# Optimization experiments

Hardware: AMD Instinct MI355X
Metric: run time of the kernel (lower is better)

The kernel has to match this reference:

```python
import jax, jax.numpy as jnp
import numpy as np

N = 131072   # utterances
D = 256      # embedding dim
C = 1024     # speakers (unique labels)


def setup_inputs() -> dict:
    key = jax.random.key(0)
    k1, k2 = jax.random.split(key)
    embeddings = jax.random.normal(k1, (N, D), dtype=jnp.float32)
    labels = jax.random.randint(k2, (N,), 0, C, dtype=jnp.int32)
    w = jnp.asarray(10.0, dtype=jnp.float32)
    b = jnp.asarray(-5.0, dtype=jnp.float32)
    return {"embeddings": embeddings, "labels": labels, "w": w, "b": b}


def reference(embeddings, labels, w, b):
    # Segment mean -> centroids [C, D]. With N >> C all labels occur, so
    # torch.unique(labels) == arange(C) and target == labels.
    sums = jax.ops.segment_sum(embeddings, labels, num_segments=C)
    counts = jax.ops.segment_sum(jnp.ones((embeddings.shape[0],), embeddings.dtype),
                                 labels, num_segments=C)
    centroids = sums / counts[:, None]
    # logits [N, C]
    logits = w * jnp.einsum('nd,cd->nc', embeddings, centroids) + b
    logp = jax.nn.log_softmax(logits, axis=-1)
    nll = -jnp.take_along_axis(logp, labels[:, None].astype(jnp.int32), axis=1)[:, 0]
    return jnp.mean(nll)
```

## Files before the change

### kernel.cpp

```cpp
#include <hip/hip_runtime.h>
#include <hip/hip_bf16.h>

#define NROWS 131072
#define DDIM  256
#define CDIM  1024

#define L2E 1.4426950408889634f
#define LN2 0.6931471805599453f

typedef short bf16x8 __attribute__((ext_vector_type(8)));
typedef float f32x4 __attribute__((ext_vector_type(4)));

__device__ __forceinline__ unsigned short f2b(float x) {
    unsigned int u = __builtin_bit_cast(unsigned int, x);
    u = (u + 0x7FFFu + ((u >> 16) & 1u)) >> 16;
    return (unsigned short)u;
}

__global__ void k_hist(const int* __restrict__ labels, int* __restrict__ hist) {
    const int i = blockIdx.x * 256 + threadIdx.x;
    atomicAdd(&hist[labels[i]], 1);
}

__global__ void k_scan(const int* __restrict__ hist, int* __restrict__ offsets) {
    __shared__ int tmp[CDIM];
    const int t = threadIdx.x;
    const int v = hist[t];
    tmp[t] = v;
    __syncthreads();
    for (int d = 1; d < CDIM; d <<= 1) {
        const int add = (t >= d) ? tmp[t - d] : 0;
        __syncthreads();
        tmp[t] += add;
        __syncthreads();
    }
    offsets[t] = tmp[t] - v;
    if (t == CDIM - 1) offsets[CDIM] = tmp[t];
}

__global__ void k_scatter(const int* __restrict__ labels, const int* __restrict__ offsets,
                          int* __restrict__ cursor, int* __restrict__ rowidx) {
    const int i = blockIdx.x * 256 + threadIdx.x;
    const int lab = labels[i];
    const int pos = atomicAdd(&cursor[lab], 1);
    rowidx[offsets[lab] + pos] = i;
}

__global__ void k_centroid(const float* __restrict__ emb, const int* __restrict__ rowidx,
                           const int* __restrict__ offsets, unsigned short* __restrict__ cent) {
    __shared__ f32x4 red[4][64];
    const int c = blockIdx.x;
    const int t = threadIdx.x;
    const int w = t >> 6;
    const int lane = t & 63;
    const int beg = offsets[c], end = offsets[c + 1];

    f32x4 acc = {0.0f, 0.0f, 0.0f, 0.0f};
    for (int i = beg + w * 2; i < end; i += 8) {
        const int row0 = rowidx[i];
        const int row1 = (i + 1 < end) ? rowidx[i + 1] : -1;
        const float4 v0 = *reinterpret_cast<const float4*>(emb + (size_t)row0 * DDIM + lane * 4);
        if (row1 >= 0) {
            const float4 v1 = *reinterpret_cast<const float4*>(emb + (size_t)row1 * DDIM + lane * 4);
            acc[0] += v1.x; acc[1] += v1.y; acc[2] += v1.z; acc[3] += v1.w;
        }
        acc[0] += v0.x; acc[1] += v0.y; acc[2] += v0.z; acc[3] += v0.w;
    }
    red[w][lane] = acc;
    __syncthreads();
    if (t < 64) {
        const f32x4 a0 = red[0][t], a1 = red[1][t], a2 = red[2][t], a3 = red[3][t];
        const float inv = 1.0f / (float)(end - beg);
        ushort4 h;
        h.x = f2b((a0[0] + a1[0] + a2[0] + a3[0]) * inv);
        h.y = f2b((a0[1] + a1[1] + a2[1] + a3[1]) * inv);
        h.z = f2b((a0[2] + a1[2] + a2[2] + a3[2]) * inv);
        h.w = f2b((a0[3] + a1[3] + a2[3] + a3[3]) * inv);
        *reinterpret_cast<ushort4*>(cent + c * DDIM + t * 4) = h;
    }
}

__launch_bounds__(256, 2)
__global__ void k_logits(const float* __restrict__ emb, const int* __restrict__ labels,
                         const unsigned short* __restrict__ cent, const float* __restrict__ wp,
                         float* __restrict__ nll_accum) {
    __shared__ unsigned short A_lds[64 * 256];
    __shared__ unsigned short B_lds[64 * 256];
    char* const Ab = reinterpret_cast<char*>(A_lds);
    char* const Bb = reinterpret_cast<char*>(B_lds);

    const float wscale = wp[0];
    const int t = threadIdx.x;
    const int wave = t >> 6;
    const int lane = t & 63;
    const int lg = lane >> 4;
    const int lr = lane & 15;
    const int rowbase = blockIdx.x * 64;

    for (int i = 0; i < 16; ++i) {
        const int flat = i * 1024 + t * 4;
        const int row = flat >> 8;
        const int k = flat & 255;
        const float4 v = *reinterpret_cast<const float4*>(emb + (size_t)(rowbase + row) * DDIM + k);
        ushort4 h;
        h.x = f2b(v.x); h.y = f2b(v.y); h.z = f2b(v.z); h.w = f2b(v.w);
        const int byte = ((row << 9) + (k << 1)) ^ ((row & 7) << 4);
        *reinterpret_cast<ushort4*>(Ab + byte) = h;
    }
    __syncthreads();

    bf16x8 af[8];
    {
        const int row = wave * 16 + lr;
#pragma unroll
        for (int kk = 0; kk < 8; ++kk) {
            const int byte = ((row << 9) + kk * 64 + lg * 16) ^ ((row & 7) << 4);
            af[kk] = *reinterpret_cast<const bf16x8*>(Ab + byte);
        }
    }

    float m[4], s[4], lv[4];
    int labs[4];
#pragma unroll
    for (int r = 0; r < 4; ++r) {
        m[r] = -1e30f; s[r] = 0.0f; lv[r] = 0.0f;
        labs[r] = labels[rowbase + wave * 16 + lg * 4 + r];
    }

    for (int cc = 0; cc < 16; ++cc) {
        __syncthreads();
        const unsigned short* src = cent + cc * (64 * 256);
        for (int i = 0; i < 8; ++i) {
            const int flat = i * 2048 + t * 8;
            const int col = flat >> 8;
            const int k = flat & 255;
            const uint4 v = *reinterpret_cast<const uint4*>(src + flat);
            const int byte = ((col << 9) + (k << 1)) ^ ((col & 7) << 4);
            *reinterpret_cast<uint4*>(Bb + byte) = v;
        }
        __syncthreads();

        float vals[4][4];
#pragma unroll
        for (int ct = 0; ct < 4; ++ct) {
            f32x4 acc = {0.0f, 0.0f, 0.0f, 0.0f};
            const int brow = ct * 16 + lr;
#pragma unroll
            for (int kk = 0; kk < 8; ++kk) {
                const int byte = ((brow << 9) + kk * 64 + lg * 16) ^ ((brow & 7) << 4);
                const bf16x8 bf = *reinterpret_cast<const bf16x8*>(Bb + byte);
                acc = __builtin_amdgcn_mfma_f32_16x16x32_bf16(af[kk], bf, acc, 0, 0, 0);
            }
            const int colg = cc * 64 + ct * 16 + lr;
#pragma unroll
            for (int r = 0; r < 4; ++r) {
                const float v = wscale * acc[r];
                vals[ct][r] = v;
                if (colg == labs[r]) lv[r] = v;
            }
        }
#pragma unroll
        for (int r = 0; r < 4; ++r) {
            const float cmax = fmaxf(fmaxf(vals[0][r], vals[1][r]),
                                     fmaxf(vals[2][r], vals[3][r]));
            const float mo = m[r];
            const float mn = fmaxf(mo, cmax);
            const float ssum = exp2f((vals[0][r] - mn) * L2E) + exp2f((vals[1][r] - mn) * L2E)
                             + exp2f((vals[2][r] - mn) * L2E) + exp2f((vals[3][r] - mn) * L2E);
            s[r] = s[r] * exp2f((mo - mn) * L2E) + ssum;
            m[r] = mn;
        }
    }

    float part = 0.0f;
#pragma unroll
    for (int r = 0; r < 4; ++r) {
        float mm = m[r], ss = s[r], ll = lv[r];
#pragma unroll
        for (int off = 1; off < 16; off <<= 1) {
            const float mo = __shfl_xor(mm, off, 64);
            const float so = __shfl_xor(ss, off, 64);
            const float lo = __shfl_xor(ll, off, 64);
            const float mn = fmaxf(mm, mo);
            ss = ss * exp2f((mm - mn) * L2E) + so * exp2f((mo - mn) * L2E);
            mm = mn;
            ll += lo;
        }
        if (lr == 0) {
            const float lse = mm + log2f(ss) * LN2;
            part += (lse - ll);
        }
    }
    if (lr == 0) atomicAdd(nll_accum, part * (1.0f / NROWS));
}

__global__ void k_final(const float* __restrict__ accum, float* __restrict__ out) {
    out[0] = accum[0];
}

extern "C" void kernel_launch(void* const* d_in, const int* in_sizes, int n_in,
                              void* d_out, int out_size, void* d_ws, size_t ws_size,
                              hipStream_t stream) {
    const float* emb = (const float*)d_in[0];
    const int* labels = (const int*)d_in[1];
    const float* wp = (const float*)d_in[2];
    float* out = (float*)d_out;

    int* hist = (int*)d_ws;
    int* cursor = (int*)((char*)d_ws + 4096);
    int* offsets = (int*)((char*)d_ws + 8192);
    float* accum = (float*)((char*)d_ws + 12544);
    int* rowidx = (int*)((char*)d_ws + 16384);
    unsigned short* cent = (unsigned short*)((char*)d_ws + 540672);

    hipMemsetAsync(d_ws, 0, 16384, stream);

    k_hist<<<NROWS / 256, 256, 0, stream>>>(labels, hist);
    k_scan<<<1, CDIM, 0, stream>>>(hist, offsets);
    k_scatter<<<NROWS / 256, 256, 0, stream>>>(labels, offsets, cursor, rowidx);
    k_centroid<<<CDIM, 256, 0, stream>>>(emb, rowidx, offsets, cent);
    k_logits<<<NROWS / 64, 256, 0, stream>>>(emb, labels, cent, wp, accum);
    k_final<<<1, 1, 0, stream>>>(accum, out);
}
```

Before: 488.1 us.

## Fuse label prep into one kernel and double-buffer pre-swizzled centroids via async LDS loads

Merges histogram, scan and scatter into a single 1024-thread block using LDS atomics. This removes the memset and several launches, and k_final is dropped by accumulating straight into the output. Centroids are now written in an MFMA-fragment-ready layout, so k_logits can stream them with global_load_lds straight into a double-buffered LDS tile, overlapping the next chunk's load with the current MFMAs. The risk is that the single-block prep kernel serialises 131K labels on one CU.

```diff
diff --git a/kernel.cpp b/kernel.cpp
--- a/kernel.cpp
+++ b/kernel.cpp
@@ -10,6 +10,10 @@
 
 typedef short bf16x8 __attribute__((ext_vector_type(8)));
 typedef float f32x4 __attribute__((ext_vector_type(4)));
+
+#define GLOAD_LDS16(g, l) __builtin_amdgcn_global_load_lds( \
+    (const __attribute__((address_space(1))) void*)(g),      \
+    (__attribute__((address_space(3))) void*)(l), 16, 0, 0)
 
 __device__ __forceinline__ unsigned short f2b(float x) {
     unsigned int u = __builtin_bit_cast(unsigned int, x);
@@ -17,43 +21,54 @@
     return (unsigned short)u;
 }
 
-__global__ void k_hist(const int* __restrict__ labels, int* __restrict__ hist) {
-    const int i = blockIdx.x * 256 + threadIdx.x;
-    atomicAdd(&hist[labels[i]], 1);
-}
-
-__global__ void k_scan(const int* __restrict__ hist, int* __restrict__ offsets) {
-    __shared__ int tmp[CDIM];
+__global__ void k_prep(const int* __restrict__ labels, int* __restrict__ offsets,
+                       int* __restrict__ rowidx, float* __restrict__ out) {
+    __shared__ int h[CDIM];
+    __shared__ int c[CDIM];
     const int t = threadIdx.x;
-    const int v = hist[t];
-    tmp[t] = v;
+    h[t] = 0;
+    __syncthreads();
+    const int4* l4 = (const int4*)labels;
+    for (int i = t; i < NROWS / 4; i += 1024) {
+        const int4 v = l4[i];
+        atomicAdd(&h[v.x], 1); atomicAdd(&h[v.y], 1);
+        atomicAdd(&h[v.z], 1); atomicAdd(&h[v.w], 1);
+    }
+    __syncthreads();
+    const int v = h[t];
+    c[t] = v;
     __syncthreads();
     for (int d = 1; d < CDIM; d <<= 1) {
-        const int add = (t >= d) ? tmp[t - d] : 0;
+        const int add = (t >= d) ? c[t - d] : 0;
         __syncthreads();
-        tmp[t] += add;
+        c[t] += add;
         __syncthreads();
     }
-    offsets[t] = tmp[t] - v;
-    if (t == CDIM - 1) offsets[CDIM] = tmp[t];
-}
-
-__global__ void k_scatter(const int* __restrict__ labels, const int* __restrict__ offsets,
-                          int* __restrict__ cursor, int* __restrict__ rowidx) {
-    const int i = blockIdx.x * 256 + threadIdx.x;
-    const int lab = labels[i];
-    const int pos = atomicAdd(&cursor[lab], 1);
-    rowidx[offsets[lab] + pos] = i;
+    const int excl = c[t] - v;
+    offsets[t] = excl;
+    if (t == CDIM - 1) offsets[CDIM] = c[t];
+    c[t] = excl;
+    if (t == 0) out[0] = 0.0f;
+    __syncthreads();
+    for (int i = t; i < NROWS / 4; i += 1024) {
+        const int4 v4 = l4[i];
+        const int base = i * 4;
+        int p;
+        p = atomicAdd(&c[v4.x], 1); rowidx[p] = base;
+        p = atomicAdd(&c[v4.y], 1); rowidx[p] = base + 1;
+        p = atomicAdd(&c[v4.z], 1); rowidx[p] = base + 2;
+        p = atomicAdd(&c[v4.w], 1); rowidx[p] = base + 3;
+    }
 }
 
 __global__ void k_centroid(const float* __restrict__ emb, const int* __restrict__ rowidx,
-                           const int* __restrict__ offsets, unsigned short* __restrict__ cent) {
+                           const int* __restrict__ offsets, unsigned short* __restrict__ centG) {
     __shared__ f32x4 red[4][64];
-    const int c = blockIdx.x;
+    const int cgrp = blockIdx.x;
     const int t = threadIdx.x;
     const int w = t >> 6;
     const int lane = t & 63;
-    const int beg = offsets[c], end = offsets[c + 1];
+    const int beg = offsets[cgrp], end = offsets[cgrp + 1];
 
     f32x4 acc = {0.0f, 0.0f, 0.0f, 0.0f};
     for (int i = beg + w * 2; i < end; i += 8) {
@@ -68,87 +83,96 @@
     }
     red[w][lane] = acc;
     __syncthreads();
-    if (t < 64) {
-        const f32x4 a0 = red[0][t], a1 = red[1][t], a2 = red[2][t], a3 = red[3][t];
+    if (t < 32) {
         const float inv = 1.0f / (float)(end - beg);
-        ushort4 h;
-        h.x = f2b((a0[0] + a1[0] + a2[0] + a3[0]) * inv);
-        h.y = f2b((a0[1] + a1[1] + a2[1] + a3[1]) * inv);
-        h.z = f2b((a0[2] + a1[2] + a2[2] + a3[2]) * inv);
-        h.w = f2b((a0[3] + a1[3] + a2[3] + a3[3]) * inv);
-        *reinterpret_cast<ushort4*>(cent + c * DDIM + t * 4) = h;
+        f32x4 a = red[0][2 * t], b4 = red[0][2 * t + 1];
+#pragma unroll
+        for (int ww = 1; ww < 4; ++ww) {
+            const f32x4 x = red[ww][2 * t], y = red[ww][2 * t + 1];
+            a[0] += x[0]; a[1] += x[1]; a[2] += x[2]; a[3] += x[3];
+            b4[0] += y[0]; b4[1] += y[1]; b4[2] += y[2]; b4[3] += y[3];
+        }
+        uint4 u;
+        u.x = (unsigned)f2b(a[0] * inv) | ((unsigned)f2b(a[1] * inv) << 16);
+        u.y = (unsigned)f2b(a[2] * inv) | ((unsigned)f2b(a[3] * inv) << 16);
+        u.z = (unsigned)f2b(b4[0] * inv) | ((unsigned)f2b(b4[1] * inv) << 16);
+        u.w = (unsigned)f2b(b4[2] * inv) | ((unsigned)f2b(b4[3] * inv) << 16);
+        const int cc = cgrp >> 6, ctq = (cgrp >> 4) & 3, lr2 = cgrp & 15;
+        const int kk = t >> 2, lg2 = t & 3;
+        *reinterpret_cast<uint4*>(centG + (size_t)cc * 16384 + ctq * 4096 + kk * 512
+                                  + (lg2 * 16 + lr2) * 8) = u;
     }
 }
 
 __launch_bounds__(256, 2)
 __global__ void k_logits(const float* __restrict__ emb, const int* __restrict__ labels,
-                         const unsigned short* __restrict__ cent, const float* __restrict__ wp,
-                         float* __restrict__ nll_accum) {
-    __shared__ unsigned short A_lds[64 * 256];
-    __shared__ unsigned short B_lds[64 * 256];
-    char* const Ab = reinterpret_cast<char*>(A_lds);
-    char* const Bb = reinterpret_cast<char*>(B_lds);
+                         const unsigned short* __restrict__ centG, const float* __restrict__ wp,
+                         float* __restrict__ out) {
+    __shared__ unsigned short lds[2][16384];
+    char* const Ab = reinterpret_cast<char*>(&lds[0][0]);
 
     const float wscale = wp[0];
     const int t = threadIdx.x;
-    const int wave = t >> 6;
+    const int w = t >> 6;
     const int lane = t & 63;
     const int lg = lane >> 4;
     const int lr = lane & 15;
     const int rowbase = blockIdx.x * 64;
+
+#pragma unroll
+    for (int j = 0; j < 8; ++j) {
+        const int J = w * 8 + j;
+        GLOAD_LDS16(centG + J * 512 + lane * 8, &lds[1][J * 512]);
+    }
 
     for (int i = 0; i < 16; ++i) {
         const int flat = i * 1024 + t * 4;
         const int row = flat >> 8;
         const int k = flat & 255;
         const float4 v = *reinterpret_cast<const float4*>(emb + (size_t)(rowbase + row) * DDIM + k);
-        ushort4 h;
-        h.x = f2b(v.x); h.y = f2b(v.y); h.z = f2b(v.z); h.w = f2b(v.w);
+        ushort4 hh;
+        hh.x = f2b(v.x); hh.y = f2b(v.y); hh.z = f2b(v.z); hh.w = f2b(v.w);
         const int byte = ((row << 9) + (k << 1)) ^ ((row & 7) << 4);
-        *reinterpret_cast<ushort4*>(Ab + byte) = h;
+        *reinterpret_cast<ushort4*>(Ab + byte) = hh;
     }
     __syncthreads();
 
     bf16x8 af[8];
     {
-        const int row = wave * 16 + lr;
+        const int row = w * 16 + lr;
 #pragma unroll
         for (int kk = 0; kk < 8; ++kk) {
             const int byte = ((row << 9) + kk * 64 + lg * 16) ^ ((row & 7) << 4);
             af[kk] = *reinterpret_cast<const bf16x8*>(Ab + byte);
         }
     }
+    __syncthreads();
 
     float m[4], s[4], lv[4];
     int labs[4];
 #pragma unroll
     for (int r = 0; r < 4; ++r) {
         m[r] = -1e30f; s[r] = 0.0f; lv[r] = 0.0f;
-        labs[r] = labels[rowbase + wave * 16 + lg * 4 + r];
+        labs[r] = labels[rowbase + w * 16 + lg * 4 + r];
     }
 
     for (int cc = 0; cc < 16; ++cc) {
-        __syncthreads();
-        const unsigned short* src = cent + cc * (64 * 256);
-        for (int i = 0; i < 8; ++i) {
-            const int flat = i * 2048 + t * 8;
-            const int col = flat >> 8;
-            const int k = flat & 255;
-            const uint4 v = *reinterpret_cast<const uint4*>(src + flat);
-            const int byte = ((col << 9) + (k << 1)) ^ ((col & 7) << 4);
-            *reinterpret_cast<uint4*>(Bb + byte) = v;
-        }
-        __syncthreads();
-
+        if (cc < 15) {
+            const unsigned short* src = centG + (cc + 1) * 16384;
+#pragma unroll
+            for (int j = 0; j < 8; ++j) {
+                const int J = w * 8 + j;
+                GLOAD_LDS16(src + J * 512 + lane * 8, &lds[cc & 1][J * 512]);
+            }
+        }
+        const unsigned short* bb = &lds[(cc + 1) & 1][lane * 8];
         float vals[4][4];
 #pragma unroll
         for (int ct = 0; ct < 4; ++ct) {
             f32x4 acc = {0.0f, 0.0f, 0.0f, 0.0f};
-            const int brow = ct * 16 + lr;
 #pragma unroll
             for (int kk = 0; kk < 8; ++kk) {
-                const int byte = ((brow << 9) + kk * 64 + lg * 16) ^ ((brow & 7) << 4);
-                const bf16x8 bf = *reinterpret_cast<const bf16x8*>(Bb + byte);
+                const bf16x8 bf = *reinterpret_cast<const bf16x8*>(bb + ct * 4096 + kk * 512);
                 acc = __builtin_amdgcn_mfma_f32_16x16x32_bf16(af[kk], bf, acc, 0, 0, 0);
             }
             const int colg = cc * 64 + ct * 16 + lr;
@@ -170,6 +194,7 @@
             s[r] = s[r] * exp2f((mo - mn) * L2E) + ssum;
             m[r] = mn;
         }
+        __syncthreads();
     }
 
     float part = 0.0f;
@@ -191,11 +216,7 @@
             part += (lse - ll);
         }
     }
-    if (lr == 0) atomicAdd(nll_accum, part * (1.0f / NROWS));
-}
-
-__global__ void k_final(const float* __restrict__ accum, float* __restrict__ out) {
-    out[0] = accum[0];
+    if (lr == 0) atomicAdd(out, part * (1.0f / NROWS));
 }
 
 extern "C" void kernel_launch(void* const* d_in, const int* in_sizes, int n_in,
@@ -206,19 +227,11 @@
     const float* wp = (const float*)d_in[2];
     float* out = (float*)d_out;
 
-    int* hist = (int*)d_ws;
-    int* cursor = (int*)((char*)d_ws + 4096);
-    int* offsets = (int*)((char*)d_ws + 8192);
-    float* accum = (float*)((char*)d_ws + 12544);
-    int* rowidx = (int*)((char*)d_ws + 16384);
-    unsigned short* cent = (unsigned short*)((char*)d_ws + 540672);
-
-    hipMemsetAsync(d_ws, 0, 16384, stream);
-
-    k_hist<<<NROWS / 256, 256, 0, stream>>>(labels, hist);
-    k_scan<<<1, CDIM, 0, stream>>>(hist, offsets);
-    k_scatter<<<NROWS / 256, 256, 0, stream>>>(labels, offsets, cursor, rowidx);
-    k_centroid<<<CDIM, 256, 0, stream>>>(emb, rowidx, offsets, cent);
-    k_logits<<<NROWS / 64, 256, 0, stream>>>(emb, labels, cent, wp, accum);
-    k_final<<<1, 1, 0, stream>>>(accum, out);
-}
+    int* offsets = (int*)d_ws;
+    int* rowidx = (int*)((char*)d_ws + 8192);
+    unsigned short* centG = (unsigned short*)((char*)d_ws + 532480);
+
+    k_prep<<<1, 1024, 0, stream>>>(labels, offsets, rowidx, out);
+    k_centroid<<<CDIM, 256, 0, stream>>>(emb, rowidx, offsets, centG);
+    k_logits<<<NROWS / 64, 256, 0, stream>>>(emb, labels, centG, wp, out);
+}
```

Result: faster. 456.5 us (-6.5%).
